# Performance work log

Measured on AMD Instinct MI355X. Metric: run time of the kernel, lower is better.

## Reference

```python
import jax, jax.numpy as jnp
import numpy as np

B, N, DIM = 4, 1024, 768
HEADS, DIM_HEAD = 12, 64
INNER = HEADS * DIM_HEAD  # 768
SCALE = DIM ** -0.5


def setup_inputs() -> dict:
    key = jax.random.key(0)
    ks = jax.random.split(key, 5)
    return {
        "x": jax.random.normal(ks[0], (B, N, DIM), dtype=jnp.float32),
        "pos_embedding": jax.random.normal(ks[1], (B, N, DIM), dtype=jnp.float32),
        "w_qkv": jax.random.normal(ks[2], (DIM, 3 * INNER), dtype=jnp.float32) * (DIM ** -0.5),
        "w_qk_pos": jax.random.normal(ks[3], (DIM, 2 * INNER), dtype=jnp.float32) * (DIM ** -0.5),
        "w_out": jax.random.normal(ks[4], (INNER, DIM), dtype=jnp.float32) * (INNER ** -0.5),
        "b_out": jnp.zeros((DIM,), dtype=jnp.float32),
    }


def _split_heads(t):
    # [b, n, h*d] -> [b, h, n, d]
    b, n, _ = t.shape
    return t.reshape(b, n, HEADS, DIM_HEAD).transpose(0, 2, 1, 3)


def reference(x, pos_embedding, w_qkv, w_qk_pos, w_out, b_out):
    qkv = x @ w_qkv  # [b, n, 3*inner]
    q, k, v = (_split_heads(t) for t in jnp.split(qkv, 3, axis=-1))
    qk_pos = pos_embedding @ w_qk_pos  # [b, n, 2*inner]
    q_pos, k_pos = (_split_heads(t) for t in jnp.split(qk_pos, 2, axis=-1))

    dots = jnp.einsum('bhid,bhjd->bhij', q, k) * SCALE
    dots_pos = jnp.einsum('bhid,bhjd->bhij', q_pos, k_pos) * SCALE
    dots = (dots + dots_pos) * 0.5  # averaged content+positional scores

    attn = jax.nn.softmax(dots, axis=-1)
    out = jnp.einsum('bhij,bhjd->bhid', attn, v)
    out = out.transpose(0, 2, 1, 3).reshape(x.shape[0], x.shape[1], INNER)
    return out @ w_out + b_out
```

## Files before the change

kernel.cpp:

```cpp
#include <hip/hip_runtime.h>
#include <cstdint>
#include <cstddef>

typedef __bf16 bf16;
typedef __bf16 bf16x8 __attribute__((ext_vector_type(8)));
typedef __bf16 bf16x4v __attribute__((ext_vector_type(4)));
typedef float  f32x4  __attribute__((ext_vector_type(4)));

#define MFMA(a, b, c) __builtin_amdgcn_mfma_f32_16x16x32_bf16((a), (b), (c), 0, 0, 0)

typedef __attribute__((address_space(3))) unsigned int  lds_u32;
typedef __attribute__((address_space(1))) unsigned int glob_u32;


__global__ void k_prep(const float* __restrict__ x, const float* __restrict__ pos,
                       const float* __restrict__ w_qkv, const float* __restrict__ w_qk_pos,
                       const float* __restrict__ w_out,
                       bf16* __restrict__ xb, bf16* __restrict__ posb,
                       bf16* __restrict__ wqkvT, bf16* __restrict__ wqkposT,
                       bf16* __restrict__ woutT) {
    __shared__ float t[32][33];
    const int blk = blockIdx.x;
    if (blk < 6144) {
        int i = blk * 256 + threadIdx.x;
        const float* in = x; bf16* out = xb;
        if (i >= 786432) { i -= 786432; in = pos; out = posb; }
        float4 v = reinterpret_cast<const float4*>(in)[i];
        bf16x4v o; o[0] = (bf16)v.x; o[1] = (bf16)v.y; o[2] = (bf16)v.z; o[3] = (bf16)v.w;
        reinterpret_cast<bf16x4v*>(out)[i] = o;
        return;
    }
    int bx = (blk - 6144) % 144, ky = (blk - 6144) / 144;
    const float* in; bf16* out; int N;
    if (bx < 72)       { in = w_qkv;    out = wqkvT;   N = 2304; }
    else if (bx < 120) { in = w_qk_pos; out = wqkposT; N = 1536; bx -= 72; }
    else               { in = w_out;    out = woutT;   N = 768;  bx -= 120; }
    const int n0 = bx * 32, k0 = ky * 32;
    const int tx = threadIdx.x & 31, ty = threadIdx.x >> 5;
#pragma unroll
    for (int r = 0; r < 32; r += 8)
        t[ty + r][tx] = in[(size_t)(k0 + ty + r) * N + n0 + tx];
    __syncthreads();
#pragma unroll
    for (int r = 0; r < 32; r += 8)
        out[(size_t)(n0 + ty + r) * 768 + k0 + tx] = (bf16)t[tx][ty + r];
}

__launch_bounds__(256, 3)
__global__ void k_gemm12(const bf16* __restrict__ xb, const bf16* __restrict__ posb,
                         const bf16* __restrict__ wqkvT, const bf16* __restrict__ wqkposT,
                         bf16* __restrict__ qcat, bf16* __restrict__ kcat,
                         bf16* __restrict__ vT) {
    __shared__ bf16 lA[2][128][32];
    __shared__ bf16 lB[2][128][32];

    const int tid  = threadIdx.x;
    const int lane = tid & 63, wave = tid >> 6;
    const int quad = lane >> 4, col = lane & 15;
    const int sw2  = (col >> 1) & 3;
    const int wm = (wave >> 1) * 64, wn = (wave & 1) * 64;

    const int fid = blockIdx.x;
    const int xcd = fid & 7, s = fid >> 3;
    const int sx = s % 15, sy = s / 15;
    int bx = (xcd & 1) * 15 + sx;
    const int by = (xcd >> 1) * 8 + sy;

    int mode, nBase;
    const bf16 *A, *BT;
    if (bx < 18) { mode = 0; A = xb;   BT = wqkvT;   nBase = bx * 128; }
    else         { mode = 1; A = posb; BT = wqkposT; nBase = (bx - 18) * 128; }
    const int mBase = by * 128;

    const bf16* Ap = A  + (size_t)mBase * 768;
    const bf16* Bp = BT + (size_t)nBase * 768;

#define STAGE12(buf, k0)                                                        \
    _Pragma("unroll")                                                           \
    for (int j = 0; j < 2; ++j) {                                               \
        int idx = (wave * 2 + j) * 64 + lane;                                   \
        int row = idx >> 2, c = (idx & 3) ^ ((row >> 1) & 3);                   \
        __builtin_amdgcn_global_load_lds(                                       \
            (const glob_u32*)(Ap + (size_t)row * 768 + (k0) + c * 8),           \
            (lds_u32*)((char*)&lA[buf][0][0] + (wave * 2 + j) * 1024), 16, 0, 0);\
        __builtin_amdgcn_global_load_lds(                                       \
            (const glob_u32*)(Bp + (size_t)row * 768 + (k0) + c * 8),           \
            (lds_u32*)((char*)&lB[buf][0][0] + (wave * 2 + j) * 1024), 16, 0, 0);\
    }

    f32x4 acc[4][4];
#pragma unroll
    for (int mi = 0; mi < 4; ++mi)
#pragma unroll
        for (int ni = 0; ni < 4; ++ni) acc[mi][ni] = f32x4{0.f, 0.f, 0.f, 0.f};

    STAGE12(0, 0)
    for (int it = 0; it < 24; ++it) {
        const int cur = it & 1, nxt = cur ^ 1;
        __syncthreads();
        if (it < 23) STAGE12(nxt, (it + 1) * 32)

        bf16x8 af[4], bfg[4];
#pragma unroll
        for (int mi = 0; mi < 4; ++mi)
            af[mi]  = *(const bf16x8*)&lA[cur][wm + mi * 16 + col][(quad ^ sw2) * 8];
#pragma unroll
        for (int ni = 0; ni < 4; ++ni)
            bfg[ni] = *(const bf16x8*)&lB[cur][wn + ni * 16 + col][(quad ^ sw2) * 8];
#pragma unroll
        for (int mi = 0; mi < 4; ++mi)
#pragma unroll
            for (int ni = 0; ni < 4; ++ni)
                acc[mi][ni] = MFMA(af[mi], bfg[ni], acc[mi][ni]);
    }
#undef STAGE12

    const float c2s = 0.018042195912f * 1.44269504089f;
    const int bb = mBase >> 10;
    const int sr0 = (mBase & 1023) + wm + quad * 4;
#pragma unroll
    for (int ni = 0; ni < 4; ++ni) {
        const int nb = nBase + wn + ni * 16;
        const int which = (mode == 0) ? (nb >= 1536 ? 2 : (nb >= 768 ? 1 : 0))
                                      : (nb >= 768 ? 1 : 0);
        const int rem = nb - which * 768;
        const int hh = rem >> 6, dd0 = rem & 63;
        const size_t hb = (size_t)(bb * 12 + hh);
        if (mode == 0 && which == 2) {
            bf16* dstv = vT + (hb * 64 + dd0 + col) * 1024 + sr0;
#pragma unroll
            for (int mi = 0; mi < 4; ++mi) {
                bf16x4v pk;
#pragma unroll
                for (int r = 0; r < 4; ++r) pk[r] = (bf16)acc[mi][ni][r];
                *(bf16x4v*)(dstv + mi * 16) = pk;
            }
        } else {
            const float scl = (which == 0) ? c2s : 1.0f;
            bf16* dstq = (which == 0 ? qcat : kcat)
                       + (hb * 1024 + sr0) * 128 + (mode == 1 ? 64 : 0) + dd0 + col;
#pragma unroll
            for (int mi = 0; mi < 4; ++mi)
#pragma unroll
                for (int r = 0; r < 4; ++r)
                    dstq[(size_t)(mi * 16 + r) * 128] = (bf16)(acc[mi][ni][r] * scl);
        }
    }
}

__launch_bounds__(256, 3)
__global__ void k_attn(const bf16* __restrict__ qcat, const bf16* __restrict__ kcat,
                       const bf16* __restrict__ vT, bf16* __restrict__ attn_out) {
    __shared__ bf16 lK[2][64][128];
    __shared__ bf16 lV[2][64][64];

    const int tid  = threadIdx.x;
    const int lane = tid & 63, wave = tid >> 6;
    const int quad = lane >> 4, col = lane & 15;
    const int sw   = col & 7;
    const int q01  = quad >> 1, qlo = quad & 1;

    const int fid = blockIdx.x;
    const int xcd = fid & 7, s = fid >> 3;
    const int qt = s & 15;
    const int unit = (s >> 4) * 8 + xcd;
    const int b = unit / 12, h = unit % 12;

    const bf16* Qb = qcat + (size_t)unit * 1024 * 128;
    const bf16* Kb = kcat + (size_t)unit * 1024 * 128;
    const bf16* Vb = vT   + (size_t)unit * 64 * 1024;

    const int kidx = wave * 256 + lane;
    const int vidx = wave * 128 + lane;

#define STAGE_K(buf, kv0)                                                      \
    _Pragma("unroll")                                                          \
    for (int j = 0; j < 4; ++j) {                                              \
        int idx = kidx + j * 64;                                               \
        int row = idx >> 4, c = idx & 15, csrc = c ^ (row & 7);                \
        __builtin_amdgcn_global_load_lds(                                      \
            (const glob_u32*)(Kb + (size_t)((kv0) + row) * 128 + csrc * 8),    \
            (lds_u32*)(&lK[buf][0][0] + (wave * 4 + j) * 512), 16, 0, 0);      \
    }
#define STAGE_V(buf, kv0)                                                      \
    _Pragma("unroll")                                                          \
    for (int j = 0; j < 2; ++j) {                                              \
        int idx = vidx + j * 64;                                               \
        int row = idx >> 3, c = idx & 7, csrc = c ^ (row & 7);                 \
        __builtin_amdgcn_global_load_lds(                                      \
            (const glob_u32*)(Vb + (size_t)row * 1024 + (kv0) + csrc * 8),     \
            (lds_u32*)(&lV[buf][0][0] + (wave * 2 + j) * 512), 16, 0, 0);      \
    }

    bf16x8 qb[4];
    {
        const bf16* qrow = Qb + (size_t)(qt * 64 + wave * 16 + col) * 128;
#pragma unroll
        for (int f = 0; f < 4; ++f) qb[f] = *(const bf16x8*)(qrow + f * 32 + quad * 8);
    }

    f32x4 o[4];
#pragma unroll
    for (int vt = 0; vt < 4; ++vt) o[vt] = f32x4{0.f, 0.f, 0.f, 0.f};
    float lsum = 0.f;

    STAGE_K(0, 0)
    STAGE_V(0, 0)

    for (int it = 0; it < 16; ++it) {
        const int cur = it & 1, nxt = cur ^ 1;
        __syncthreads();
        if (it < 15) {
            const int kv1 = (it + 1) * 64;
            STAGE_K(nxt, kv1)
            STAGE_V(nxt, kv1)
        }

        f32x4 st[4];
#pragma unroll
        for (int t = 0; t < 4; ++t) st[t] = f32x4{0.f, 0.f, 0.f, 0.f};
#pragma unroll
        for (int t = 0; t < 4; ++t)
#pragma unroll
            for (int f = 0; f < 4; ++f) {
                bf16x8 kf = *(const bf16x8*)&lK[cur][t * 16 + col][((f * 4 + quad) ^ sw) * 8];
                st[t] = MFMA(kf, qb[f], st[t]);
            }

        bf16x8 pbf[2];
#pragma unroll
        for (int c = 0; c < 2; ++c) {
#pragma unroll
            for (int r = 0; r < 4; ++r) {
                float p0 = exp2f(st[2 * c][r]);
                float p1 = exp2f(st[2 * c + 1][r]);
                lsum += p0 + p1;
                pbf[c][r]     = (bf16)p0;
                pbf[c][4 + r] = (bf16)p1;
            }
        }

#pragma unroll
        for (int c = 0; c < 2; ++c)
#pragma unroll
            for (int vt = 0; vt < 4; ++vt) {
                const bf16* vrow = &lV[cur][vt * 16 + col][0];
                bf16x4v va = *(const bf16x4v*)(vrow + ((c * 4 + q01) ^ sw) * 8 + qlo * 4);
                bf16x4v vb = *(const bf16x4v*)(vrow + ((c * 4 + 2 + q01) ^ sw) * 8 + qlo * 4);
                bf16x8 vf;
#pragma unroll
                for (int i = 0; i < 4; ++i) { vf[i] = va[i]; vf[4 + i] = vb[i]; }
                o[vt] = MFMA(vf, pbf[c], o[vt]);
            }
    }

    float l = lsum;
    l += __shfl_xor(l, 16, 64);
    l += __shfl_xor(l, 32, 64);
    const float inv = 1.f / l;

    const int qrow = qt * 64 + wave * 16 + col;
    bf16* dst = attn_out + ((size_t)b * 1024 + qrow) * 768 + h * 64;
#pragma unroll
    for (int vt = 0; vt < 4; ++vt)
#pragma unroll
        for (int r = 0; r < 4; ++r)
            dst[vt * 16 + quad * 4 + r] = (bf16)(o[vt][r] * inv);
#undef STAGE_K
#undef STAGE_V
}

__launch_bounds__(256, 3)
__global__ void k_gemm_out(const bf16* __restrict__ aout, const bf16* __restrict__ woutT,
                           const float* __restrict__ bias, float* __restrict__ out) {
    __shared__ bf16 lA[2][128][32];
    __shared__ bf16 lB[2][64][32];

    const int tid  = threadIdx.x;
    const int lane = tid & 63, wave = tid >> 6;
    const int quad = lane >> 4, col = lane & 15;
    const int sw2  = (col >> 1) & 3;
    const int wm = (wave >> 1) * 64, wn = (wave & 1) * 32;

    const int fid = blockIdx.x;
    const int xcd = fid & 7, s = fid >> 3;
    const int sx = s % 6, sy = s / 6;
    const int bx = (xcd & 1) * 6 + sx;
    const int by = (xcd >> 1) * 8 + sy;

    const int mBase = by * 128, nBase = bx * 64;

    const bf16* Ap = aout  + (size_t)mBase * 768;
    const bf16* Bp = woutT + (size_t)nBase * 768;

#define STAGE_O(buf, k0)                                                        \
    _Pragma("unroll")                                                           \
    for (int j = 0; j < 2; ++j) {                                               \
        int idx = (wave * 2 + j) * 64 + lane;                                   \
        int row = idx >> 2, c = (idx & 3) ^ ((row >> 1) & 3);                   \
        __builtin_amdgcn_global_load_lds(                                       \
            (const glob_u32*)(Ap + (size_t)row * 768 + (k0) + c * 8),           \
            (lds_u32*)((char*)&lA[buf][0][0] + (wave * 2 + j) * 1024), 16, 0, 0);\
    }                                                                           \
    {                                                                           \
        int idx = wave * 64 + lane;                                             \
        int row = idx >> 2, c = (idx & 3) ^ ((row >> 1) & 3);                   \
        __builtin_amdgcn_global_load_lds(                                       \
            (const glob_u32*)(Bp + (size_t)row * 768 + (k0) + c * 8),           \
            (lds_u32*)((char*)&lB[buf][0][0] + wave * 1024), 16, 0, 0);         \
    }

    f32x4 acc[4][2];
#pragma unroll
    for (int mi = 0; mi < 4; ++mi)
#pragma unroll
        for (int ni = 0; ni < 2; ++ni) acc[mi][ni] = f32x4{0.f, 0.f, 0.f, 0.f};

    STAGE_O(0, 0)
    for (int it = 0; it < 24; ++it) {
        const int cur = it & 1, nxt = cur ^ 1;
        __syncthreads();
        if (it < 23) STAGE_O(nxt, (it + 1) * 32)

        bf16x8 af[4], bfg[2];
#pragma unroll
        for (int mi = 0; mi < 4; ++mi)
            af[mi]  = *(const bf16x8*)&lA[cur][wm + mi * 16 + col][(quad ^ sw2) * 8];
#pragma unroll
        for (int ni = 0; ni < 2; ++ni)
            bfg[ni] = *(const bf16x8*)&lB[cur][wn + ni * 16 + col][(quad ^ sw2) * 8];
#pragma unroll
        for (int mi = 0; mi < 4; ++mi)
#pragma unroll
            for (int ni = 0; ni < 2; ++ni)
                acc[mi][ni] = MFMA(af[mi], bfg[ni], acc[mi][ni]);
    }
#undef STAGE_O

#pragma unroll
    for (int mi = 0; mi < 4; ++mi)
#pragma unroll
        for (int ni = 0; ni < 2; ++ni)
#pragma unroll
            for (int r = 0; r < 4; ++r) {
                int m = mBase + wm + mi * 16 + quad * 4 + r;
                int n = nBase + wn + ni * 16 + col;
                out[(size_t)m * 768 + n] = acc[mi][ni][r] + bias[n];
            }
}

extern "C" void kernel_launch(void* const* d_in, const int* in_sizes, int n_in,
                              void* d_out, int out_size, void* d_ws, size_t ws_size,
                              hipStream_t stream) {
    const float* x        = (const float*)d_in[0];
    const float* pos      = (const float*)d_in[1];
    const float* w_qkv    = (const float*)d_in[2];
    const float* w_qk_pos = (const float*)d_in[3];
    const float* w_out    = (const float*)d_in[4];
    const float* b_out    = (const float*)d_in[5];
    float* out = (float*)d_out;

    char* ws = (char*)d_ws;
    bf16* xb      = (bf16*)(ws);
    bf16* posb    = (bf16*)(ws + 6291456);
    bf16* wqkvT   = (bf16*)(ws + 12582912);
    bf16* wqkposT = (bf16*)(ws + 16121856);
    bf16* woutT   = (bf16*)(ws + 18481152);
    bf16* qcat    = (bf16*)(ws + 19660800);
    bf16* kcat    = (bf16*)(ws + 32243712);
    bf16* vT      = (bf16*)(ws + 44826624);
    bf16* aout    = (bf16*)(ws + 51118080);

    k_prep<<<9600, 256, 0, stream>>>(x, pos, w_qkv, w_qk_pos, w_out,
                                     xb, posb, wqkvT, wqkposT, woutT);
    k_gemm12<<<960, 256, 0, stream>>>(xb, posb, wqkvT, wqkposT, qcat, kcat, vT);
    k_attn<<<768, 256, 0, stream>>>(qcat, kcat, vT, aout);
    k_gemm_out<<<384, 256, 0, stream>>>(aout, woutT, b_out, out);
}
```

Measured before the change: 178.6 us.

## Stage V via registers with padded permuted LDS layout, shrink out-GEMM tiles

```diff
diff --git a/kernel.cpp b/kernel.cpp
--- a/kernel.cpp
+++ b/kernel.cpp
@@ -152,13 +152,12 @@
 __global__ void k_attn(const bf16* __restrict__ qcat, const bf16* __restrict__ kcat,
                        const bf16* __restrict__ vT, bf16* __restrict__ attn_out) {
     __shared__ bf16 lK[2][64][128];
-    __shared__ bf16 lV[2][64][64];
+    __shared__ bf16 lV[2][64][72];
 
     const int tid  = threadIdx.x;
     const int lane = tid & 63, wave = tid >> 6;
     const int quad = lane >> 4, col = lane & 15;
     const int sw   = col & 7;
-    const int q01  = quad >> 1, qlo = quad & 1;
 
     const int fid = blockIdx.x;
     const int xcd = fid & 7, s = fid >> 3;
@@ -171,7 +170,6 @@
     const bf16* Vb = vT   + (size_t)unit * 64 * 1024;
 
     const int kidx = wave * 256 + lane;
-    const int vidx = wave * 128 + lane;
 
 #define STAGE_K(buf, kv0)                                                      \
     _Pragma("unroll")                                                          \
@@ -182,14 +180,26 @@
             (const glob_u32*)(Kb + (size_t)((kv0) + row) * 128 + csrc * 8),    \
             (lds_u32*)(&lK[buf][0][0] + (wave * 4 + j) * 512), 16, 0, 0);      \
     }
-#define STAGE_V(buf, kv0)                                                      \
+
+    int vdj[2], vsk[2], vka[2];
+#pragma unroll
+    for (int j = 0; j < 2; ++j) {
+        int cid = wave * 128 + j * 64 + lane;
+        vdj[j] = cid >> 3;
+        int sck = cid & 7;
+        vsk[j] = sck * 8;
+        vka[j] = (sck >> 2) * 32 + (sck & 1) * 16 + ((sck >> 1) & 1) * 4;
+    }
+
+#define LOAD_V(kv0)                                                            \
+    _Pragma("unroll")                                                          \
+    for (int j = 0; j < 2; ++j)                                                \
+        vreg[j] = *(const uint4*)(Vb + (size_t)vdj[j] * 1024 + (kv0) + vsk[j]);
+#define WRITE_V(buf)                                                           \
     _Pragma("unroll")                                                          \
     for (int j = 0; j < 2; ++j) {                                              \
-        int idx = vidx + j * 64;                                               \
-        int row = idx >> 3, c = idx & 7, csrc = c ^ (row & 7);                 \
-        __builtin_amdgcn_global_load_lds(                                      \
-            (const glob_u32*)(Vb + (size_t)row * 1024 + (kv0) + csrc * 8),     \
-            (lds_u32*)(&lV[buf][0][0] + (wave * 2 + j) * 512), 16, 0, 0);      \
+        *(uint2*)&lV[buf][vdj[j]][vka[j]]     = make_uint2(vreg[j].x, vreg[j].y);\
+        *(uint2*)&lV[buf][vdj[j]][vka[j] + 8] = make_uint2(vreg[j].z, vreg[j].w);\
     }
 
     bf16x8 qb[4];
@@ -204,8 +214,10 @@
     for (int vt = 0; vt < 4; ++vt) o[vt] = f32x4{0.f, 0.f, 0.f, 0.f};
     float lsum = 0.f;
 
+    uint4 vreg[2];
     STAGE_K(0, 0)
-    STAGE_V(0, 0)
+    LOAD_V(0)
+    WRITE_V(0)
 
     for (int it = 0; it < 16; ++it) {
         const int cur = it & 1, nxt = cur ^ 1;
@@ -213,7 +225,7 @@
         if (it < 15) {
             const int kv1 = (it + 1) * 64;
             STAGE_K(nxt, kv1)
-            STAGE_V(nxt, kv1)
+            LOAD_V(kv1)
         }
 
         f32x4 st[4];
@@ -244,14 +256,11 @@
         for (int c = 0; c < 2; ++c)
 #pragma unroll
             for (int vt = 0; vt < 4; ++vt) {
-                const bf16* vrow = &lV[cur][vt * 16 + col][0];
-                bf16x4v va = *(const bf16x4v*)(vrow + ((c * 4 + q01) ^ sw) * 8 + qlo * 4);
-                bf16x4v vb = *(const bf16x4v*)(vrow + ((c * 4 + 2 + q01) ^ sw) * 8 + qlo * 4);
-                bf16x8 vf;
-#pragma unroll
-                for (int i = 0; i < 4; ++i) { vf[i] = va[i]; vf[4 + i] = vb[i]; }
+                bf16x8 vf = *(const bf16x8*)&lV[cur][vt * 16 + col][c * 32 + quad * 8];
                 o[vt] = MFMA(vf, pbf[c], o[vt]);
             }
+
+        if (it < 15) WRITE_V(nxt)
     }
 
     float l = lsum;
@@ -262,57 +271,54 @@
     const int qrow = qt * 64 + wave * 16 + col;
     bf16* dst = attn_out + ((size_t)b * 1024 + qrow) * 768 + h * 64;
 #pragma unroll
-    for (int vt = 0; vt < 4; ++vt)
-#pragma unroll
-        for (int r = 0; r < 4; ++r)
-            dst[vt * 16 + quad * 4 + r] = (bf16)(o[vt][r] * inv);
+    for (int vt = 0; vt < 4; ++vt) {
+        bf16x4v pk;
+#pragma unroll
+        for (int r = 0; r < 4; ++r) pk[r] = (bf16)(o[vt][r] * inv);
+        *(bf16x4v*)(dst + vt * 16 + quad * 4) = pk;
+    }
 #undef STAGE_K
-#undef STAGE_V
+#undef LOAD_V
+#undef WRITE_V
 }
 
 __launch_bounds__(256, 3)
 __global__ void k_gemm_out(const bf16* __restrict__ aout, const bf16* __restrict__ woutT,
                            const float* __restrict__ bias, float* __restrict__ out) {
-    __shared__ bf16 lA[2][128][32];
+    __shared__ bf16 lA[2][64][32];
     __shared__ bf16 lB[2][64][32];
 
     const int tid  = threadIdx.x;
     const int lane = tid & 63, wave = tid >> 6;
     const int quad = lane >> 4, col = lane & 15;
     const int sw2  = (col >> 1) & 3;
-    const int wm = (wave >> 1) * 64, wn = (wave & 1) * 32;
+    const int wm = (wave >> 1) * 32, wn = (wave & 1) * 32;
 
     const int fid = blockIdx.x;
     const int xcd = fid & 7, s = fid >> 3;
-    const int sx = s % 6, sy = s / 6;
-    const int bx = (xcd & 1) * 6 + sx;
-    const int by = (xcd >> 1) * 8 + sy;
-
-    const int mBase = by * 128, nBase = bx * 64;
+    const int bx = s % 12;
+    const int by = xcd * 8 + s / 12;
+
+    const int mBase = by * 64, nBase = bx * 64;
 
     const bf16* Ap = aout  + (size_t)mBase * 768;
     const bf16* Bp = woutT + (size_t)nBase * 768;
 
 #define STAGE_O(buf, k0)                                                        \
-    _Pragma("unroll")                                                           \
-    for (int j = 0; j < 2; ++j) {                                               \
-        int idx = (wave * 2 + j) * 64 + lane;                                   \
-        int row = idx >> 2, c = (idx & 3) ^ ((row >> 1) & 3);                   \
-        __builtin_amdgcn_global_load_lds(                                       \
-            (const glob_u32*)(Ap + (size_t)row * 768 + (k0) + c * 8),           \
-            (lds_u32*)((char*)&lA[buf][0][0] + (wave * 2 + j) * 1024), 16, 0, 0);\
-    }                                                                           \
     {                                                                           \
         int idx = wave * 64 + lane;                                             \
         int row = idx >> 2, c = (idx & 3) ^ ((row >> 1) & 3);                   \
         __builtin_amdgcn_global_load_lds(                                       \
+            (const glob_u32*)(Ap + (size_t)row * 768 + (k0) + c * 8),           \
+            (lds_u32*)((char*)&lA[buf][0][0] + wave * 1024), 16, 0, 0);         \
+        __builtin_amdgcn_global_load_lds(                                       \
             (const glob_u32*)(Bp + (size_t)row * 768 + (k0) + c * 8),           \
             (lds_u32*)((char*)&lB[buf][0][0] + wave * 1024), 16, 0, 0);         \
     }
 
-    f32x4 acc[4][2];
-#pragma unroll
-    for (int mi = 0; mi < 4; ++mi)
+    f32x4 acc[2][2];
+#pragma unroll
+    for (int mi = 0; mi < 2; ++mi)
 #pragma unroll
         for (int ni = 0; ni < 2; ++ni) acc[mi][ni] = f32x4{0.f, 0.f, 0.f, 0.f};
 
@@ -322,15 +328,15 @@
         __syncthreads();
         if (it < 23) STAGE_O(nxt, (it + 1) * 32)
 
-        bf16x8 af[4], bfg[2];
-#pragma unroll
-        for (int mi = 0; mi < 4; ++mi)
+        bf16x8 af[2], bfg[2];
+#pragma unroll
+        for (int mi = 0; mi < 2; ++mi)
             af[mi]  = *(const bf16x8*)&lA[cur][wm + mi * 16 + col][(quad ^ sw2) * 8];
 #pragma unroll
         for (int ni = 0; ni < 2; ++ni)
             bfg[ni] = *(const bf16x8*)&lB[cur][wn + ni * 16 + col][(quad ^ sw2) * 8];
 #pragma unroll
-        for (int mi = 0; mi < 4; ++mi)
+        for (int mi = 0; mi < 2; ++mi)
 #pragma unroll
             for (int ni = 0; ni < 2; ++ni)
                 acc[mi][ni] = MFMA(af[mi], bfg[ni], acc[mi][ni]);
@@ -338,7 +344,7 @@
 #undef STAGE_O
 
 #pragma unroll
-    for (int mi = 0; mi < 4; ++mi)
+    for (int mi = 0; mi < 2; ++mi)
 #pragma unroll
         for (int ni = 0; ni < 2; ++ni)
 #pragma unroll
@@ -375,5 +381,5 @@
                                      xb, posb, wqkvT, wqkposT, woutT);
     k_gemm12<<<960, 256, 0, stream>>>(xb, posb, wqkvT, wqkposT, qcat, kcat, vT);
     k_attn<<<768, 256, 0, stream>>>(qcat, kcat, vT, aout);
-    k_gemm_out<<<384, 256, 0, stream>>>(aout, woutT, b_out, out);
-}
+    k_gemm_out<<<768, 256, 0, stream>>>(aout, woutT, b_out, out);
+}
```

Measured after the change: 174.4 us, median of 2. -2.3%, faster.
